# Kernel optimization log

Measured on AMD Instinct MI355X. Metric: run time of the kernel, lower is better.

## Reference

```python
import jax, jax.numpy as jnp
import numpy as np

B, EMB, P, K = 8192, 768, 96, 256
D = EMB // P  # dsub = 8


def setup_inputs() -> dict:
    key = jax.random.key(0)
    k1, k2 = jax.random.split(key)
    vecs = jax.random.normal(k1, (B, EMB), dtype=jnp.float32)
    # torch init: uniform(-1, 1)
    codebook = jax.random.uniform(k2, (P, K, D), dtype=jnp.float32, minval=-1.0, maxval=1.0)
    return {"vecs": vecs, "codebook": codebook}


def reference(vecs, codebook):
    b = vecs.shape[0]
    p, k, d = codebook.shape
    v = vecs.reshape(b, p, d)                                  # [B,P,D]
    # squared distances via expanded quadratic (avoids [B,P,K,D] broadcast):
    # ||v-c||^2 = ||v||^2 - 2 v.c + ||c||^2
    dots = jnp.einsum('bpd,pkd->bpk', v, codebook)             # [B,P,K]
    d2 = (jnp.sum(v * v, axis=-1, keepdims=True)               # [B,P,1]
          - 2.0 * dots
          + jnp.sum(codebook * codebook, axis=-1)[None])       # [1,P,K]
    proba = jax.nn.softmax(-d2, axis=-1)                       # [B,P,K]
    # straight-through hard assignment
    idx = jnp.argmax(proba, axis=-1)                           # [B,P]
    hard = jax.nn.one_hot(idx, k, dtype=proba.dtype)           # [B,P,K]
    ste = jax.lax.stop_gradient(hard - proba) + proba
    # reconstruct from codebook
    out = jnp.einsum('bpk,pkd->bpd', ste, codebook).reshape(b, p * d)
    return out
```

## Files before the change

### kernel.cpp

```cpp
#include <hip/hip_runtime.h>


typedef float f32x2 __attribute__((ext_vector_type(2)));
typedef float f32x4 __attribute__((ext_vector_type(4)));

#define TPB 256
#define KBQ 4
#define CHUNK 4

namespace {
constexpr int kB   = 8192;
constexpr int kEMB = 768;
constexpr int kP   = 96;
constexpr int kK   = 256;
constexpr int kD   = 8;
}

__device__ __forceinline__ f32x2 pk_fma(f32x2 a, f32x2 b, f32x2 c) {
    f32x2 d;
    asm("v_pk_fma_f32 %0, %1, %2, %3" : "=v"(d) : "v"(a), "v"(b), "v"(c));
    return d;
}

__device__ __forceinline__ float code_score(const f32x2* cp, const f32x2* vs,
                                            f32x2 c2z) {
    f32x2 a = pk_fma(cp[0], vs[0], c2z);
    a = pk_fma(cp[1], vs[1], a);
    a = pk_fma(cp[2], vs[2], a);
    a = pk_fma(cp[3], vs[3], a);
    return a.x + a.y;
}

__global__ __launch_bounds__(TPB, 3)
void pq_argmin_kernel(const float* __restrict__ vecs,
                      const float* __restrict__ codebook,
                      float* __restrict__ out)
{
    __shared__ alignas(16) float lds_code[kK][kD];
    __shared__ alignas(16) f32x2 lds_c2z[kK];

    const int p = blockIdx.y;
    const int t = threadIdx.x;

    {
        const f32x4* cb = reinterpret_cast<const f32x4*>(
            codebook + (size_t)p * kK * kD);
        f32x4 a = cb[2 * t];
        f32x4 b = cb[2 * t + 1];
        float c2 = a.x * a.x + a.y * a.y + a.z * a.z + a.w * a.w +
                   b.x * b.x + b.y * b.y + b.z * b.z + b.w * b.w;
        f32x4* lc = reinterpret_cast<f32x4*>(&lds_code[t][0]);
        lc[0] = a;
        lc[1] = b;
        lds_c2z[t] = f32x2{c2, 0.0f};
    }
    __syncthreads();

    const int b0 = blockIdx.x * (TPB * KBQ) + t;
    f32x2 vs[KBQ][4];
#pragma unroll
    for (int q = 0; q < KBQ; ++q) {
        const f32x4* vp = reinterpret_cast<const f32x4*>(
            vecs + (size_t)(b0 + q * TPB) * kEMB + p * kD);
        f32x4 x = vp[0];
        f32x4 y = vp[1];
        vs[q][0] = f32x2{-2.0f * x.x, -2.0f * x.y};
        vs[q][1] = f32x2{-2.0f * x.z, -2.0f * x.w};
        vs[q][2] = f32x2{-2.0f * y.x, -2.0f * y.y};
        vs[q][3] = f32x2{-2.0f * y.z, -2.0f * y.w};
    }

    float best[KBQ];
    int   bch[KBQ];
#pragma unroll
    for (int q = 0; q < KBQ; ++q) {
        best[q] = __builtin_inff();
        bch[q] = 0;
    }

#pragma unroll 2
    for (int ch = 0; ch < kK / CHUNK; ++ch) {
        f32x2 cp[CHUNK][4];
        f32x2 c2z[CHUNK];
        {
            const f32x2* zz = &lds_c2z[ch * CHUNK];
#pragma unroll
            for (int c = 0; c < CHUNK; ++c) {
                const f32x2* cc = reinterpret_cast<const f32x2*>(
                    &lds_code[ch * CHUNK + c][0]);
                cp[c][0] = cc[0]; cp[c][1] = cc[1];
                cp[c][2] = cc[2]; cp[c][3] = cc[3];
                c2z[c] = zz[c];
            }
        }
#pragma unroll
        for (int q = 0; q < KBQ; ++q) {
            float s0 = code_score(cp[0], vs[q], c2z[0]);
            float s1 = code_score(cp[1], vs[q], c2z[1]);
            float s2 = code_score(cp[2], vs[q], c2z[2]);
            float s3 = code_score(cp[3], vs[q], c2z[3]);
            float m = fminf(fminf(fminf(s0, s1), s2), s3);
            if (m < best[q]) {
                best[q] = m;
                bch[q] = ch;
            }
        }
    }

#pragma unroll
    for (int q = 0; q < KBQ; ++q) {
        const int base = bch[q] * CHUNK;
        float s[CHUNK];
#pragma unroll
        for (int c = 0; c < CHUNK; ++c) {
            f32x2 cp[4];
            const f32x2* cc = reinterpret_cast<const f32x2*>(
                &lds_code[base + c][0]);
            cp[0] = cc[0]; cp[1] = cc[1]; cp[2] = cc[2]; cp[3] = cc[3];
            s[c] = code_score(cp, vs[q], lds_c2z[base + c]);
        }
        int idx = base;
        bool fnd = (s[0] == best[q]);
#pragma unroll
        for (int c = 1; c < CHUNK; ++c) {
            bool e = (s[c] == best[q]) && !fnd;
            idx = e ? base + c : idx;
            fnd = fnd || (s[c] == best[q]);
        }
        const f32x4* row = reinterpret_cast<const f32x4*>(&lds_code[idx][0]);
        f32x4 r0 = row[0];
        f32x4 r1 = row[1];
        f32x4* op = reinterpret_cast<f32x4*>(
            out + (size_t)(b0 + q * TPB) * kEMB + p * kD);
        op[0] = r0;
        op[1] = r1;
    }
}

extern "C" void kernel_launch(void* const* d_in, const int* in_sizes, int n_in,
                              void* d_out, int out_size, void* d_ws, size_t ws_size,
                              hipStream_t stream)
{
    const float* vecs     = (const float*)d_in[0];
    const float* codebook = (const float*)d_in[1];
    float* out            = (float*)d_out;

    dim3 grid(kB / (TPB * KBQ), kP, 1);
    dim3 block(TPB, 1, 1);
    hipLaunchKernelGGL(pq_argmin_kernel, grid, block, 0, stream,
                       vecs, codebook, out);
}
```

Before: 128.4 us.

## Read codebook directly from global memory instead of staging in LDS

Removes the LDS staging of the codebook and its squared norms, so codes are loaded uniformly from global memory (likely scalar loads via the constant cache) and norms are recomputed per chunk. The chunk size doubles to 8, and the inline-asm packed FMA is replaced by plain fmaf pairs that the compiler may or may not pack. This drops the block-wide sync and LDS traffic but adds per-chunk norm recomputation and relies on scalar/cached loads for the codebook.

```diff
diff --git a/kernel.cpp b/kernel.cpp
--- a/kernel.cpp
+++ b/kernel.cpp
@@ -6,7 +6,7 @@
 
 #define TPB 256
 #define KBQ 4
-#define CHUNK 4
+#define CHUNK 8
 
 namespace {
 constexpr int kB   = 8192;
@@ -16,18 +16,27 @@
 constexpr int kD   = 8;
 }
 
-__device__ __forceinline__ f32x2 pk_fma(f32x2 a, f32x2 b, f32x2 c) {
+__device__ __forceinline__ f32x2 vfma2(f32x2 a, f32x2 b, f32x2 c) {
     f32x2 d;
-    asm("v_pk_fma_f32 %0, %1, %2, %3" : "=v"(d) : "v"(a), "v"(b), "v"(c));
+    d.x = fmaf(a.x, b.x, c.x);
+    d.y = fmaf(a.y, b.y, c.y);
     return d;
 }
 
-__device__ __forceinline__ float code_score(const f32x2* cp, const f32x2* vs,
-                                            f32x2 c2z) {
-    f32x2 a = pk_fma(cp[0], vs[0], c2z);
-    a = pk_fma(cp[1], vs[1], a);
-    a = pk_fma(cp[2], vs[2], a);
-    a = pk_fma(cp[3], vs[3], a);
+__device__ __forceinline__ float code_c2(const f32x2 c[4]) {
+    f32x2 t = c[0] * c[0];
+    t = vfma2(c[1], c[1], t);
+    t = vfma2(c[2], c[2], t);
+    t = vfma2(c[3], c[3], t);
+    return t.x + t.y;
+}
+
+__device__ __forceinline__ float code_score(const f32x2 c[4], const f32x2 vs[4],
+                                            float c2) {
+    f32x2 a = vfma2(c[0], vs[0], f32x2{c2, 0.0f});
+    a = vfma2(c[1], vs[1], a);
+    a = vfma2(c[2], vs[2], a);
+    a = vfma2(c[3], vs[3], a);
     return a.x + a.y;
 }
 
@@ -36,25 +45,10 @@
                       const float* __restrict__ codebook,
                       float* __restrict__ out)
 {
-    __shared__ alignas(16) float lds_code[kK][kD];
-    __shared__ alignas(16) f32x2 lds_c2z[kK];
-
     const int p = blockIdx.y;
     const int t = threadIdx.x;
 
-    {
-        const f32x4* cb = reinterpret_cast<const f32x4*>(
-            codebook + (size_t)p * kK * kD);
-        f32x4 a = cb[2 * t];
-        f32x4 b = cb[2 * t + 1];
-        float c2 = a.x * a.x + a.y * a.y + a.z * a.z + a.w * a.w +
-                   b.x * b.x + b.y * b.y + b.z * b.z + b.w * b.w;
-        f32x4* lc = reinterpret_cast<f32x4*>(&lds_code[t][0]);
-        lc[0] = a;
-        lc[1] = b;
-        lds_c2z[t] = f32x2{c2, 0.0f};
-    }
-    __syncthreads();
+    const float* __restrict__ cbp = codebook + (size_t)p * kK * kD;
 
     const int b0 = blockIdx.x * (TPB * KBQ) + t;
     f32x2 vs[KBQ][4];
@@ -81,25 +75,31 @@
 #pragma unroll 2
     for (int ch = 0; ch < kK / CHUNK; ++ch) {
         f32x2 cp[CHUNK][4];
-        f32x2 c2z[CHUNK];
-        {
-            const f32x2* zz = &lds_c2z[ch * CHUNK];
+        float c2[CHUNK];
 #pragma unroll
-            for (int c = 0; c < CHUNK; ++c) {
-                const f32x2* cc = reinterpret_cast<const f32x2*>(
-                    &lds_code[ch * CHUNK + c][0]);
-                cp[c][0] = cc[0]; cp[c][1] = cc[1];
-                cp[c][2] = cc[2]; cp[c][3] = cc[3];
-                c2z[c] = zz[c];
-            }
+        for (int c = 0; c < CHUNK; ++c) {
+            const f32x2* cc = reinterpret_cast<const f32x2*>(
+                cbp + (ch * CHUNK + c) * kD);
+#pragma unroll
+            for (int j = 0; j < 4; ++j) cp[c][j] = cc[j];
         }
 #pragma unroll
+        for (int c = 0; c < CHUNK; ++c) c2[c] = code_c2(cp[c]);
+
+#pragma unroll
         for (int q = 0; q < KBQ; ++q) {
-            float s0 = code_score(cp[0], vs[q], c2z[0]);
-            float s1 = code_score(cp[1], vs[q], c2z[1]);
-            float s2 = code_score(cp[2], vs[q], c2z[2]);
-            float s3 = code_score(cp[3], vs[q], c2z[3]);
-            float m = fminf(fminf(fminf(s0, s1), s2), s3);
+            float s0 = code_score(cp[0], vs[q], c2[0]);
+            float s1 = code_score(cp[1], vs[q], c2[1]);
+            float s2 = code_score(cp[2], vs[q], c2[2]);
+            float s3 = code_score(cp[3], vs[q], c2[3]);
+            float s4 = code_score(cp[4], vs[q], c2[4]);
+            float s5 = code_score(cp[5], vs[q], c2[5]);
+            float s6 = code_score(cp[6], vs[q], c2[6]);
+            float s7 = code_score(cp[7], vs[q], c2[7]);
+            float m1 = fminf(fminf(s0, s1), s2);
+            float m2 = fminf(fminf(s3, s4), s5);
+            float m3 = fminf(fminf(s6, s7), m1);
+            float m  = fminf(m2, m3);
             if (m < best[q]) {
                 best[q] = m;
                 bch[q] = ch;
@@ -113,11 +113,12 @@
         float s[CHUNK];
 #pragma unroll
         for (int c = 0; c < CHUNK; ++c) {
-            f32x2 cp[4];
-            const f32x2* cc = reinterpret_cast<const f32x2*>(
-                &lds_code[base + c][0]);
-            cp[0] = cc[0]; cp[1] = cc[1]; cp[2] = cc[2]; cp[3] = cc[3];
-            s[c] = code_score(cp, vs[q], lds_c2z[base + c]);
+            f32x2 cc[4];
+            const f32x2* src = reinterpret_cast<const f32x2*>(
+                cbp + (base + c) * kD);
+#pragma unroll
+            for (int j = 0; j < 4; ++j) cc[j] = src[j];
+            s[c] = code_score(cc, vs[q], code_c2(cc));
         }
         int idx = base;
         bool fnd = (s[0] == best[q]);
@@ -127,7 +128,7 @@
             idx = e ? base + c : idx;
             fnd = fnd || (s[c] == best[q]);
         }
-        const f32x4* row = reinterpret_cast<const f32x4*>(&lds_code[idx][0]);
+        const f32x4* row = reinterpret_cast<const f32x4*>(cbp + idx * kD);
         f32x4 r0 = row[0];
         f32x4 r1 = row[1];
         f32x4* op = reinterpret_cast<f32x4*>(
```

New measurement: 142.2 us. +10.7%, slower.

## Interleave codebook pairs so packed FMA scores two codes per lane

Applied to the files above, without the earlier changes.

The codebook is stored in LDS with pairs of codes interleaved by dimension, and each vector component is broadcast into both halves of a packed register. Each v_pk_fma_f32 now accumulates the scores of two codes at once, which removes the horizontal add per code score. Block size drops to 128 threads, each handling 8 rows for more reuse of every LDS load. The final rescoring and the output gather now read the codebook from global memory instead of LDS, and the larger per-thread state raises register pressure and may lower occupancy.

```diff
diff --git a/kernel.cpp b/kernel.cpp
--- a/kernel.cpp
+++ b/kernel.cpp
@@ -4,9 +4,8 @@
 typedef float f32x2 __attribute__((ext_vector_type(2)));
 typedef float f32x4 __attribute__((ext_vector_type(4)));
 
-#define TPB 256
-#define KBQ 4
-#define CHUNK 4
+#define TPB 128
+#define KBQ 8
 
 namespace {
 constexpr int kB   = 8192;
@@ -14,6 +13,8 @@
 constexpr int kP   = 96;
 constexpr int kK   = 256;
 constexpr int kD   = 8;
+constexpr int kNP  = kK / 2;
+constexpr int kNCH = kK / 4;
 }
 
 __device__ __forceinline__ f32x2 pk_fma(f32x2 a, f32x2 b, f32x2 c) {
@@ -22,53 +23,60 @@
     return d;
 }
 
-__device__ __forceinline__ float code_score(const f32x2* cp, const f32x2* vs,
-                                            f32x2 c2z) {
-    f32x2 a = pk_fma(cp[0], vs[0], c2z);
-    a = pk_fma(cp[1], vs[1], a);
-    a = pk_fma(cp[2], vs[2], a);
-    a = pk_fma(cp[3], vs[3], a);
-    return a.x + a.y;
+__device__ __forceinline__ float c2_of(f32x4 lo, f32x4 hi) {
+    float t = lo.x * lo.x;
+    t = fmaf(lo.y, lo.y, t);
+    t = fmaf(lo.z, lo.z, t);
+    t = fmaf(lo.w, lo.w, t);
+    t = fmaf(hi.x, hi.x, t);
+    t = fmaf(hi.y, hi.y, t);
+    t = fmaf(hi.z, hi.z, t);
+    t = fmaf(hi.w, hi.w, t);
+    return t;
 }
 
-__global__ __launch_bounds__(TPB, 3)
+__global__ __launch_bounds__(TPB, 2)
 void pq_argmin_kernel(const float* __restrict__ vecs,
                       const float* __restrict__ codebook,
                       float* __restrict__ out)
 {
-    __shared__ alignas(16) float lds_code[kK][kD];
-    __shared__ alignas(16) f32x2 lds_c2z[kK];
+    __shared__ alignas(16) f32x4 lds_pairs[kNP][4];
+    __shared__ alignas(16) f32x2 lds_c2[kNP];
 
     const int p = blockIdx.y;
     const int t = threadIdx.x;
+    const float* __restrict__ cbp = codebook + (size_t)p * kK * kD;
+    const f32x4* cb4 = reinterpret_cast<const f32x4*>(cbp);
 
     {
-        const f32x4* cb = reinterpret_cast<const f32x4*>(
-            codebook + (size_t)p * kK * kD);
-        f32x4 a = cb[2 * t];
-        f32x4 b = cb[2 * t + 1];
-        float c2 = a.x * a.x + a.y * a.y + a.z * a.z + a.w * a.w +
-                   b.x * b.x + b.y * b.y + b.z * b.z + b.w * b.w;
-        f32x4* lc = reinterpret_cast<f32x4*>(&lds_code[t][0]);
-        lc[0] = a;
-        lc[1] = b;
-        lds_c2z[t] = f32x2{c2, 0.0f};
+        f32x4 a0 = cb4[4 * t + 0];
+        f32x4 a1 = cb4[4 * t + 1];
+        f32x4 b0 = cb4[4 * t + 2];
+        f32x4 b1 = cb4[4 * t + 3];
+        lds_pairs[t][0] = f32x4{a0.x, b0.x, a0.y, b0.y};
+        lds_pairs[t][1] = f32x4{a0.z, b0.z, a0.w, b0.w};
+        lds_pairs[t][2] = f32x4{a1.x, b1.x, a1.y, b1.y};
+        lds_pairs[t][3] = f32x4{a1.z, b1.z, a1.w, b1.w};
+        lds_c2[t] = f32x2{c2_of(a0, a1), c2_of(b0, b1)};
     }
-    __syncthreads();
 
-    const int b0 = blockIdx.x * (TPB * KBQ) + t;
-    f32x2 vs[KBQ][4];
+    const int b0q = blockIdx.x * (TPB * KBQ) + t;
+    f32x2 vd[KBQ][kD];
 #pragma unroll
     for (int q = 0; q < KBQ; ++q) {
         const f32x4* vp = reinterpret_cast<const f32x4*>(
-            vecs + (size_t)(b0 + q * TPB) * kEMB + p * kD);
+            vecs + (size_t)(b0q + q * TPB) * kEMB + p * kD);
         f32x4 x = vp[0];
         f32x4 y = vp[1];
-        vs[q][0] = f32x2{-2.0f * x.x, -2.0f * x.y};
-        vs[q][1] = f32x2{-2.0f * x.z, -2.0f * x.w};
-        vs[q][2] = f32x2{-2.0f * y.x, -2.0f * y.y};
-        vs[q][3] = f32x2{-2.0f * y.z, -2.0f * y.w};
+        float m0 = -2.0f * x.x, m1 = -2.0f * x.y, m2 = -2.0f * x.z,
+              m3 = -2.0f * x.w, m4 = -2.0f * y.x, m5 = -2.0f * y.y,
+              m6 = -2.0f * y.z, m7 = -2.0f * y.w;
+        vd[q][0] = f32x2{m0, m0}; vd[q][1] = f32x2{m1, m1};
+        vd[q][2] = f32x2{m2, m2}; vd[q][3] = f32x2{m3, m3};
+        vd[q][4] = f32x2{m4, m4}; vd[q][5] = f32x2{m5, m5};
+        vd[q][6] = f32x2{m6, m6}; vd[q][7] = f32x2{m7, m7};
     }
+    __syncthreads();
 
     float best[KBQ];
     int   bch[KBQ];
@@ -79,27 +87,38 @@
     }
 
 #pragma unroll 2
-    for (int ch = 0; ch < kK / CHUNK; ++ch) {
-        f32x2 cp[CHUNK][4];
-        f32x2 c2z[CHUNK];
-        {
-            const f32x2* zz = &lds_c2z[ch * CHUNK];
-#pragma unroll
-            for (int c = 0; c < CHUNK; ++c) {
-                const f32x2* cc = reinterpret_cast<const f32x2*>(
-                    &lds_code[ch * CHUNK + c][0]);
-                cp[c][0] = cc[0]; cp[c][1] = cc[1];
-                cp[c][2] = cc[2]; cp[c][3] = cc[3];
-                c2z[c] = zz[c];
-            }
-        }
+    for (int ch = 0; ch < kNCH; ++ch) {
+        f32x4 p0a = lds_pairs[2 * ch][0];
+        f32x4 p0b = lds_pairs[2 * ch][1];
+        f32x4 p0c = lds_pairs[2 * ch][2];
+        f32x4 p0d = lds_pairs[2 * ch][3];
+        f32x4 p1a = lds_pairs[2 * ch + 1][0];
+        f32x4 p1b = lds_pairs[2 * ch + 1][1];
+        f32x4 p1c = lds_pairs[2 * ch + 1][2];
+        f32x4 p1d = lds_pairs[2 * ch + 1][3];
+        f32x4 cz = *reinterpret_cast<const f32x4*>(&lds_c2[2 * ch]);
+
 #pragma unroll
         for (int q = 0; q < KBQ; ++q) {
-            float s0 = code_score(cp[0], vs[q], c2z[0]);
-            float s1 = code_score(cp[1], vs[q], c2z[1]);
-            float s2 = code_score(cp[2], vs[q], c2z[2]);
-            float s3 = code_score(cp[3], vs[q], c2z[3]);
-            float m = fminf(fminf(fminf(s0, s1), s2), s3);
+            f32x2 a0 = pk_fma(p0a.xy, vd[q][0], cz.xy);
+            a0 = pk_fma(p0a.zw, vd[q][1], a0);
+            a0 = pk_fma(p0b.xy, vd[q][2], a0);
+            a0 = pk_fma(p0b.zw, vd[q][3], a0);
+            a0 = pk_fma(p0c.xy, vd[q][4], a0);
+            a0 = pk_fma(p0c.zw, vd[q][5], a0);
+            a0 = pk_fma(p0d.xy, vd[q][6], a0);
+            a0 = pk_fma(p0d.zw, vd[q][7], a0);
+
+            f32x2 a1 = pk_fma(p1a.xy, vd[q][0], cz.zw);
+            a1 = pk_fma(p1a.zw, vd[q][1], a1);
+            a1 = pk_fma(p1b.xy, vd[q][2], a1);
+            a1 = pk_fma(p1b.zw, vd[q][3], a1);
+            a1 = pk_fma(p1c.xy, vd[q][4], a1);
+            a1 = pk_fma(p1c.zw, vd[q][5], a1);
+            a1 = pk_fma(p1d.xy, vd[q][6], a1);
+            a1 = pk_fma(p1d.zw, vd[q][7], a1);
+
+            float m = fminf(fminf(fminf(a0.x, a0.y), a1.x), a1.y);
             if (m < best[q]) {
                 best[q] = m;
                 bch[q] = ch;
@@ -109,29 +128,35 @@
 
 #pragma unroll
     for (int q = 0; q < KBQ; ++q) {
-        const int base = bch[q] * CHUNK;
-        float s[CHUNK];
+        const int base = bch[q] * 4;
+        float s[4];
 #pragma unroll
-        for (int c = 0; c < CHUNK; ++c) {
-            f32x2 cp[4];
-            const f32x2* cc = reinterpret_cast<const f32x2*>(
-                &lds_code[base + c][0]);
-            cp[0] = cc[0]; cp[1] = cc[1]; cp[2] = cc[2]; cp[3] = cc[3];
-            s[c] = code_score(cp, vs[q], lds_c2z[base + c]);
+        for (int c = 0; c < 4; ++c) {
+            f32x4 lo = cb4[2 * (base + c)];
+            f32x4 hi = cb4[2 * (base + c) + 1];
+            float cc2 = c2_of(lo, hi);
+            float s_ = fmaf(lo.x, vd[q][0].x, cc2);
+            s_ = fmaf(lo.y, vd[q][1].x, s_);
+            s_ = fmaf(lo.z, vd[q][2].x, s_);
+            s_ = fmaf(lo.w, vd[q][3].x, s_);
+            s_ = fmaf(hi.x, vd[q][4].x, s_);
+            s_ = fmaf(hi.y, vd[q][5].x, s_);
+            s_ = fmaf(hi.z, vd[q][6].x, s_);
+            s_ = fmaf(hi.w, vd[q][7].x, s_);
+            s[c] = s_;
         }
         int idx = base;
         bool fnd = (s[0] == best[q]);
 #pragma unroll
-        for (int c = 1; c < CHUNK; ++c) {
+        for (int c = 1; c < 4; ++c) {
             bool e = (s[c] == best[q]) && !fnd;
             idx = e ? base + c : idx;
             fnd = fnd || (s[c] == best[q]);
         }
-        const f32x4* row = reinterpret_cast<const f32x4*>(&lds_code[idx][0]);
-        f32x4 r0 = row[0];
-        f32x4 r1 = row[1];
+        f32x4 r0 = cb4[2 * idx];
+        f32x4 r1 = cb4[2 * idx + 1];
         f32x4* op = reinterpret_cast<f32x4*>(
-            out + (size_t)(b0 + q * TPB) * kEMB + p * kD);
+            out + (size_t)(b0q + q * TPB) * kEMB + p * kD);
         op[0] = r0;
         op[1] = r1;
     }
```

Result: slower. 139.0 us (+8.3%).
